# Performance work log

Measured on AMD Instinct MI355X. Metric: run time of the kernel, lower is better.

The kernel has to match this reference:

```python
import jax, jax.numpy as jnp
import numpy as np
import math

B, S, DIM, QK, HID = 20, 500, 300, 128, 600  # batch, seq, model dim, query_key_dim, hidden_dim
ROT = 32          # rotary dim = min(32, query_key_dim)
NB, MD = 32, 128  # T5 bias num_buckets, max_distance


def _layernorm(x, g, b, eps=1e-5):
    mu = jnp.mean(x, axis=-1, keepdims=True)
    var = jnp.var(x, axis=-1, keepdims=True)
    return (x - mu) / jnp.sqrt(var + eps) * g + b


def _rowquant(y, axis):
    # per-row (or per-col) symmetric int4-range quant used by the module:
    # scale = max|y|/15, clamp to [-15,15], truncate toward zero (torch .to(int8))
    s = jnp.max(jnp.abs(y), axis=axis, keepdims=True) / 15.0
    yq = jnp.trunc(jnp.clip(y / s, -15.0, 15.0))
    return yq, s


def _rotary(t):
    # rotary-embedding-torch: rotate first ROT features, interleaved pairs
    inv_freq = 1.0 / (10000.0 ** (jnp.arange(0, ROT, 2, dtype=jnp.float32) / ROT))  # [ROT/2]
    pos = jnp.arange(S, dtype=jnp.float32)
    freqs = jnp.repeat(pos[:, None] * inv_freq[None, :], 2, axis=-1)  # [S, ROT]
    cos, sin = jnp.cos(freqs), jnp.sin(freqs)
    tr, tp = t[..., :ROT], t[..., ROT:]
    x1, x2 = tr[..., 0::2], tr[..., 1::2]
    rot_half = jnp.stack([-x2, x1], axis=-1).reshape(tr.shape)
    return jnp.concatenate([tr * cos + rot_half * sin, tp], axis=-1)


def _t5_bias(rel_emb):
    # non-causal T5 relative position bucket, num_buckets=32 -> halved to 16
    pos = jnp.arange(S)
    n = -(pos[None, :] - pos[:, None])  # -(k_pos - q_pos)
    nb = NB // 2
    ret = (n < 0).astype(jnp.int32) * nb
    n = jnp.abs(n)
    max_exact = nb // 2
    is_small = n < max_exact
    n_safe = jnp.maximum(n, 1).astype(jnp.float32)
    val_large = max_exact + (jnp.log(n_safe / max_exact) / math.log(MD / max_exact) * (nb - max_exact)).astype(jnp.int32)
    val_large = jnp.minimum(val_large, nb - 1)
    bucket = ret + jnp.where(is_small, n, val_large)  # [S, S]
    return rel_emb[bucket, 0] * math.sqrt(QK)


def setup_inputs() -> dict:
    key = jax.random.key(0)
    ks = jax.random.split(key, 16)
    nrm = lambda i, shp, std=0.02: jax.random.normal(ks[i], shp, jnp.float32) * std
    uni = lambda i, shp, lo, hi: jax.random.uniform(ks[i], shp, jnp.float32, lo, hi)
    return {
        "x": jax.random.normal(ks[0], (B, S, DIM), jnp.float32),
        "norm_gamma": jnp.ones((DIM,), jnp.float32),
        "norm_beta": jnp.zeros((DIM,), jnp.float32),
        "Wh": nrm(1, (2 * HID, DIM)),
        "bh": jnp.zeros((2 * HID,), jnp.float32),
        "Wqk": nrm(2, (QK, DIM)),
        "bqk": jnp.zeros((QK,), jnp.float32),
        "os_gamma": nrm(3, (2, QK)),
        "os_beta": jnp.zeros((2, QK), jnp.float32),
        "Wo": nrm(4, (DIM, HID)),
        "bo": jnp.zeros((DIM,), jnp.float32),
        "rel_emb": nrm(5, (NB, 1), 0.1),
        "qk_s": uni(6, (DIM,), 0.5, 1.5),
        "hidden_s": uni(7, (DIM,), 0.5, 1.5),
        "out_s": uni(8, (HID,), 0.5, 1.5),
        "hidden_params": uni(9, (2 * HID,), 0.01, 0.05),
        "qk_params": uni(10, (QK,), 0.01, 0.05),
        "out_params": uni(11, (DIM,), 0.01, 0.05),
    }


def reference(x, norm_gamma, norm_beta, Wh, bh, Wqk, bqk, os_gamma, os_beta, Wo, bo,
              rel_emb, qk_s, hidden_s, out_s, hidden_params, qk_params, out_params):
    normed = _layernorm(x, norm_gamma, norm_beta)
    # token shift on first half of features
    half = DIM // 2
    x_shift = jnp.pad(normed[..., :half], ((0, 0), (1, 0), (0, 0)))[:, :S, :]
    normed = jnp.concatenate([x_shift, normed[..., half:]], axis=-1)

    # per-weight-column pre-scale then per-row int8 quant
    xq_q, sq = _rowquant(normed / qk_s, axis=-1)      # sq [B,S,1]
    xh_q, sh = _rowquant(normed / hidden_s, axis=-1)  # sh [B,S,1]

    # to_hidden: Linear + SiLU, then dequant outer(row_scale, hidden_params)
    v_gate = jax.nn.silu(xh_q @ Wh.T + bh) * (sh * hidden_params)  # [B,S,2*HID]
    v, gate = v_gate[..., :HID], v_gate[..., HID:]

    qk = jax.nn.silu(xq_q @ Wqk.T + bqk) * (sq * qk_params)  # [B,S,QK]
    q = qk * os_gamma[0] + os_beta[0]
    k = qk * os_gamma[1] + os_beta[1]
    q, k = _rotary(q), _rotary(k)

    qq, qs = _rowquant(q, axis=-1)
    kq, ks_ = _rowquant(k, axis=-1)
    sim = jnp.trunc(jnp.einsum('bid,bjd->bij', qq, kq)) * qs * jnp.swapaxes(ks_, 1, 2)
    sim = sim + _t5_bias(rel_emb)

    attn = jnp.square(jax.nn.relu(sim / S))
    aq, as_ = _rowquant(attn, axis=-1)  # as_ [B,S,1]
    vq, vs = _rowquant(v, axis=1)       # vs [B,1,HID] (per-column)
    out = jnp.trunc(jnp.einsum('bij,bjd->bid', aq, vq)) * as_ * vs  # [B,S,HID]

    out = out * gate / out_s
    oq, osc = _rowquant(out, axis=-1)
    out = (oq @ Wo.T + bo) * (osc * out_params)  # [B,S,DIM]
    return out + x
```

## Files before the change

kernel.cpp:

```cpp
#include <hip/hip_runtime.h>
#include <math.h>

#define B_   20
#define S_   500
#define DIM_ 300
#define QK_  128
#define HID_ 600
#define NROW (B_ * S_)

typedef int   v4i  __attribute__((ext_vector_type(4)));

__device__ __forceinline__ unsigned short f32_to_bf16(float f) {
  unsigned int u = __float_as_uint(f);
  unsigned int r = (u + 0x7FFFu + ((u >> 16) & 1u)) >> 16;
  return (unsigned short)r;
}
__device__ __forceinline__ float bf16_to_f32(unsigned short s) {
  return __uint_as_float(((unsigned int)s) << 16);
}

__device__ __forceinline__ float quant15(float y, float s) {
  return truncf(fminf(fmaxf(__fdiv_rn(y, s), -15.f), 15.f));
}

__global__ __launch_bounds__(256) void k_prep_ln(
    const float* __restrict__ x,
    const float* __restrict__ g, const float* __restrict__ b,
    const float* __restrict__ qk_s, const float* __restrict__ hidden_s,
    signed char* __restrict__ xq8, signed char* __restrict__ xh8,
    float* __restrict__ sq, float* __restrict__ sh,
    const float* __restrict__ rel_emb, float* __restrict__ dbias,
    const float* __restrict__ Wh, signed char* __restrict__ q1h, float* __restrict__ s1h,
    const float* __restrict__ Wo, signed char* __restrict__ q1o, float* __restrict__ s1o,
    const float* __restrict__ Wqk, signed char* __restrict__ q1k, float* __restrict__ s1k) {
  int blk = blockIdx.x;
  int tid = threadIdx.x;
  int lane = tid & 63;
  if (blk < 2500) {
    int row = blk * 4 + (tid >> 6);
    if (row >= NROW) return;
    bool hasp = (row % S_) > 0;
    const float* xr = x + (size_t)row * DIM_;
    const float* xpr = x + (size_t)(row - 1) * DIM_;
    float xc[5], xp[5];
    #pragma unroll
    for (int i = 0; i < 5; ++i) {
      int c = lane + i * 64;
      xc[i] = (c < DIM_) ? xr[c] : 0.f;
      xp[i] = (hasp && c < DIM_) ? xpr[c] : 0.f;
    }
    float sc = 0.f, sp = 0.f;
    #pragma unroll
    for (int i = 0; i < 5; ++i) { sc += xc[i]; sp += xp[i]; }
    #pragma unroll
    for (int off = 1; off < 64; off <<= 1) {
      sc += __shfl_xor(sc, off);
      sp += __shfl_xor(sp, off);
    }
    float mu_c = sc / (float)DIM_, mu_p = sp / (float)DIM_;
    float vc = 0.f, vp = 0.f;
    #pragma unroll
    for (int i = 0; i < 5; ++i) {
      int c = lane + i * 64;
      if (c < DIM_) {
        float dc = xc[i] - mu_c; vc += dc * dc;
        float dp = xp[i] - mu_p; vp += dp * dp;
      }
    }
    #pragma unroll
    for (int off = 1; off < 64; off <<= 1) {
      vc += __shfl_xor(vc, off);
      vp += __shfl_xor(vp, off);
    }
    float den_c = sqrtf(vc / (float)DIM_ + 1e-5f);
    float den_p = sqrtf(vp / (float)DIM_ + 1e-5f);
    float yq[5], yh[5];
    float mq = 0.f, mh = 0.f;
    #pragma unroll
    for (int i = 0; i < 5; ++i) {
      int c = lane + i * 64;
      if (c < DIM_) {
        float src;
        if (c < DIM_ / 2)
          src = hasp ? __fdiv_rn(xp[i] - mu_p, den_p) * g[c] + b[c] : 0.f;
        else
          src = __fdiv_rn(xc[i] - mu_c, den_c) * g[c] + b[c];
        yq[i] = __fdiv_rn(src, qk_s[c]);
        yh[i] = __fdiv_rn(src, hidden_s[c]);
        mq = fmaxf(mq, fabsf(yq[i]));
        mh = fmaxf(mh, fabsf(yh[i]));
      }
    }
    #pragma unroll
    for (int off = 1; off < 64; off <<= 1) {
      mq = fmaxf(mq, __shfl_xor(mq, off));
      mh = fmaxf(mh, __shfl_xor(mh, off));
    }
    float sqv = mq / 15.0f, shv = mh / 15.0f;
    if (lane == 0) { sq[row] = sqv; sh[row] = shv; }
    #pragma unroll
    for (int i = 0; i < 5; ++i) {
      int c = lane + i * 64;
      if (c < DIM_) {
        xq8[(size_t)row * 320 + c] = (signed char)quant15(yq[i], sqv);
        xh8[(size_t)row * 320 + c] = (signed char)quant15(yh[i], shv);
      } else if (c < 320) {
        xq8[(size_t)row * 320 + c] = 0;
        xh8[(size_t)row * 320 + c] = 0;
      }
    }
    return;
  }
  int jidx = (blk - 2500) * 4 + (tid >> 6);
  if (jidx >= 1744) return;
  if (jidx < 16) {
    int idx = jidx * 64 + lane;
    int dd = idx - 512;
    int ret = (dd < 0) ? 16 : 0;
    int n = dd < 0 ? -dd : dd;
    int v;
    if (n < 8)       v = n;
    else if (n < 12) v = 8;
    else if (n < 16) v = 9;
    else if (n < 23) v = 10;
    else if (n < 32) v = 11;
    else if (n < 46) v = 12;
    else if (n < 64) v = 13;
    else if (n < 91) v = 14;
    else             v = 15;
    dbias[idx] = __fmul_rn(rel_emb[ret + v], 11.313708498984761f);
    return;
  }
  const float* src; signed char* q1; float* s1;
  int j, C, CP;
  if (jidx < 1296)      { j = jidx - 16;   src = Wh;  q1 = q1h; s1 = s1h; C = DIM_; CP = 320; }
  else if (jidx < 1616) { j = jidx - 1296; src = Wo;  q1 = q1o; s1 = s1o; C = HID_; CP = 640; }
  else                  { j = jidx - 1616; src = Wqk; q1 = q1k; s1 = s1k; C = DIM_; CP = 320; }
  float m = 0.f;
  for (int k = lane; k < C; k += 64) m = fmaxf(m, fabsf(src[(size_t)j * C + k]));
  #pragma unroll
  for (int off = 1; off < 64; off <<= 1) m = fmaxf(m, __shfl_xor(m, off));
  float s1v = m / 127.0f;
  float s1inv = s1v > 0.f ? 1.0f / s1v : 0.f;
  if (lane == 0) s1[j] = s1v;
  for (int k = lane; k < CP; k += 64) {
    float wv = (k < C) ? src[(size_t)j * C + k] : 0.f;
    float q1f = fminf(fmaxf(rintf(wv * s1inv), -127.f), 127.f);
    q1[(size_t)j * CP + k] = (signed char)q1f;
  }
}

__global__ __launch_bounds__(512) void k_hidden(
    const signed char* __restrict__ xh8p, const float* __restrict__ sh,
    const signed char* __restrict__ q1h, const float* __restrict__ s1h,
    const float* __restrict__ bh, const float* __restrict__ hp,
    unsigned short* __restrict__ v16, unsigned short* __restrict__ gate16,
    int* __restrict__ vsmax) {
  int j0 = blockIdx.x * 64;
  int i0 = blockIdx.y * 256;
  int tid = threadIdx.x;
  int w = tid >> 6, l = tid & 63, g = l >> 4, ln = l & 15;
  int wm = w >> 1, wn = w & 1;
  __shared__ __align__(16) signed char smem[33792];
  signed char* a_lds  = smem;
  signed char* b1_lds = smem + 16384;
  unsigned short* st  = (unsigned short*)smem;

  int r0 = tid >> 2, ch0 = tid & 3;
  int r1 = r0 + 128;
  int koff0 = ((ch0 ^ ((r0 >> 1) & 3)) * 16);
  int koff1 = ((ch0 ^ ((r1 >> 1) & 3)) * 16);
  int ga0 = i0 + r0; if (ga0 >= NROW) ga0 = NROW - 1;
  int ga1 = i0 + r1; if (ga1 >= NROW) ga1 = NROW - 1;
  const signed char* srcA0 = xh8p + (size_t)ga0 * 320 + koff0;
  const signed char* srcA1 = xh8p + (size_t)ga1 * 320 + koff1;
  bool hasB = tid < 256;
  int br = (tid & 255) >> 2, bch = tid & 3;
  int bkoff = ((bch ^ ((br >> 1) & 3)) * 16);
  const signed char* srcB = q1h + (size_t)(j0 + br) * 320 + bkoff;

  v4i pa0 = *(const v4i*)srcA0;
  v4i pa1 = *(const v4i*)srcA1;
  v4i zero = {0, 0, 0, 0};
  v4i pb = hasB ? *(const v4i*)srcB : zero;

  int rxor = ((g ^ ((ln >> 1) & 3)) * 16);
  v4i acc1[4][2];
  #pragma unroll
  for (int sl = 0; sl < 4; ++sl)
    #pragma unroll
    for (int t = 0; t < 2; ++t) acc1[sl][t] = zero;

  for (int st_i = 0; st_i < 5; ++st_i) {
    *(v4i*)(a_lds + tid * 16)        = pa0;
    *(v4i*)(a_lds + 8192 + tid * 16) = pa1;
    if (hasB) *(v4i*)(b1_lds + tid * 16) = pb;
    __syncthreads();
    if (st_i < 4) {
      int k0 = (st_i + 1) * 64;
      pa0 = *(const v4i*)(srcA0 + k0);
      pa1 = *(const v4i*)(srcA1 + k0);
      if (hasB) pb = *(const v4i*)(srcB + k0);
    }
    v4i af[4];
    #pragma unroll
    for (int sl = 0; sl < 4; ++sl)
      af[sl] = *(const v4i*)(a_lds + (wm * 64 + sl * 16 + ln) * 64 + rxor);
    #pragma unroll
    for (int t = 0; t < 2; ++t) {
      int boff = (wn * 32 + t * 16 + ln) * 64 + rxor;
      v4i b1 = *(const v4i*)(b1_lds + boff);
      #pragma unroll
      for (int sl = 0; sl < 4; ++sl)
        acc1[sl][t] = __builtin_amdgcn_mfma_i32_16x16x64_i8(af[sl], b1, acc1[sl][t], 0, 0, 0);
    }
    __syncthreads();
  }
  int rbase = i0 + wm * 64;
  int b0 = rbase / S_;
  int bbound = (b0 + 1) * S_;
  int rtop = rbase + 63; if (rtop >= NROW) rtop = NROW - 1;
  int b1i = rtop / S_;
  #pragma unroll
  for (int t = 0; t < 2; ++t) {
    int col = j0 + wn * 32 + t * 16 + ln;
    int cl = wn * 32 + t * 16 + ln;
    if (col < 2 * HID_) {
      float s1v = s1h[col], bc = bh[col], hpc = hp[col];
      bool isv = col < HID_;
      float m0 = 0.f, m1 = 0.f;
      #pragma unroll
      for (int sl = 0; sl < 4; ++sl) {
        #pragma unroll
        for (int r = 0; r < 4; ++r) {
          int grow = rbase + sl * 16 + g * 4 + r;
          if (grow < NROW) {
            float z = s1v * (float)acc1[sl][t][r] + bc;
            float sig = 1.0f / (1.0f + __expf(-z));
            float val = __fmul_rn(z * sig, __fmul_rn(sh[grow], hpc));
            unsigned short hv = f32_to_bf16(val);
            st[(wm * 64 + sl * 16 + g * 4 + r) * 66 + cl] = hv;
            if (isv) {
              float vr = fabsf(bf16_to_f32(hv));
              if (grow < bbound) m0 = fmaxf(m0, vr);
              else               m1 = fmaxf(m1, vr);
            }
          }
        }
      }
      if (isv) {
        atomicMax(&vsmax[b0 * 640 + col], __float_as_int(m0));
        if (b1i != b0) atomicMax(&vsmax[b1i * 640 + col], __float_as_int(m1));
      }
    }
  }
  __syncthreads();
  for (int idx = tid; idx < 2048; idx += 512) {
    int r = idx >> 3, seg = idx & 7;
    int grow = i0 + r;
    int col0 = j0 + seg * 8;
    if (grow < NROW && col0 < 2 * HID_) {
      const unsigned int* sp = (const unsigned int*)(st + r * 66 + seg * 8);
      v4i pk;
      pk[0] = sp[0]; pk[1] = sp[1]; pk[2] = sp[2]; pk[3] = sp[3];
      if (col0 < HID_)
        *(v4i*)(v16 + (size_t)grow * HID_ + col0) = pk;
      else
        *(v4i*)(gate16 + (size_t)grow * HID_ + (col0 - HID_)) = pk;
    }
  }
}

__global__ __launch_bounds__(256) void k_qk(
    const signed char* __restrict__ xq8p, const float* __restrict__ sq,
    const signed char* __restrict__ q1k, const float* __restrict__ s1k,
    const float* __restrict__ bqk, const float* __restrict__ qkp,
    const float* __restrict__ osg, const float* __restrict__ osb,
    signed char* __restrict__ qq8, signed char* __restrict__ kq2,
    float* __restrict__ qs, float* __restrict__ ks) {
  int i0 = blockIdx.x * 64;
  int tid = threadIdx.x;
  int w = tid >> 6, l = tid & 63, g = l >> 4, ln = l & 15;
  __shared__ __align__(16) signed char a_lds[64 * 64];
  __shared__ __align__(16) signed char b1_lds[128 * 64];
  __shared__ float freqs[32];
  if (tid < 32) {
    double e = (double)(tid & ~1) / 32.0;
    freqs[tid] = (float)(1.0 / pow(10000.0, e));
  }
  int arow = tid >> 2;
  int xorb = (((tid & 3) ^ ((tid >> 3) & 3)) * 16);
  int ga = i0 + arow; if (ga >= NROW) ga = NROW - 1;
  const signed char* srcA   = xq8p + (size_t)ga * 320 + xorb;
  const signed char* srcB1a = q1k + (size_t)arow * 320 + xorb;
  const signed char* srcB1b = q1k + (size_t)(64 + arow) * 320 + xorb;
  v4i pa   = *(const v4i*)srcA;
  v4i pb1a = *(const v4i*)srcB1a, pb1b = *(const v4i*)srcB1b;
  int rxor = ((g ^ ((ln >> 1) & 3)) * 16);
  v4i acc1[8];
  v4i zero = {0, 0, 0, 0};
  #pragma unroll
  for (int t = 0; t < 8; ++t) acc1[t] = zero;
  for (int st = 0; st < 5; ++st) {
    *(v4i*)(a_lds + tid * 16)         = pa;
    *(v4i*)(b1_lds + tid * 16)        = pb1a;
    *(v4i*)(b1_lds + 4096 + tid * 16) = pb1b;
    __syncthreads();
    if (st < 4) {
      int k0 = (st + 1) * 64;
      pa   = *(const v4i*)(srcA + k0);
      pb1a = *(const v4i*)(srcB1a + k0);
      pb1b = *(const v4i*)(srcB1b + k0);
    }
    v4i af = *(const v4i*)(a_lds + (w * 16 + ln) * 64 + rxor);
    #pragma unroll
    for (int t = 0; t < 8; ++t) {
      int boff = (t * 16 + ln) * 64 + rxor;
      v4i b1 = *(const v4i*)(b1_lds + boff);
      acc1[t] = __builtin_amdgcn_mfma_i32_16x16x64_i8(af, b1, acc1[t], 0, 0, 0);
    }
    __syncthreads();
  }
  int growr[4]; float sqr[4];
  #pragma unroll
  for (int r = 0; r < 4; ++r) {
    growr[r] = i0 + w * 16 + g * 4 + r;
    int gc = growr[r] < NROW ? growr[r] : NROW - 1;
    sqr[r] = sq[gc];
  }
  float qv[8][4], kv[8][4];
  #pragma unroll
  for (int t = 0; t < 8; ++t) {
    int c = t * 16 + ln;
    float s1v = s1k[c], bc = bqk[c], qkpc = qkp[c];
    float g0 = osg[c], g1 = osg[QK_ + c], b0 = osb[c], b1v = osb[QK_ + c];
    #pragma unroll
    for (int r = 0; r < 4; ++r) {
      float z = s1v * (float)acc1[t][r] + bc;
      float sig = 1.0f / (1.0f + expf(-z));
      float qkv = __fmul_rn(z * sig, __fmul_rn(sqr[r], qkpc));
      qv[t][r] = __fadd_rn(__fmul_rn(qkv, g0), b0);
      kv[t][r] = __fadd_rn(__fmul_rn(qkv, g1), b1v);
    }
  }
  #pragma unroll
  for (int t = 0; t < 2; ++t) {
    float inv = freqs[t * 16 + ln];
    #pragma unroll
    for (int r = 0; r < 4; ++r) {
      int pos = growr[r] % S_;
      float fr = __fmul_rn((float)pos, inv);
      float cs = cosf(fr), sn = sinf(fr);
      float qo = __shfl_xor(qv[t][r], 1);
      float ko = __shfl_xor(kv[t][r], 1);
      float rq = ((ln & 1) == 0) ? -qo : qo;
      float rk = ((ln & 1) == 0) ? -ko : ko;
      qv[t][r] = __fadd_rn(__fmul_rn(qv[t][r], cs), __fmul_rn(rq, sn));
      kv[t][r] = __fadd_rn(__fmul_rn(kv[t][r], cs), __fmul_rn(rk, sn));
    }
  }
  float qsv[4], ksv[4];
  #pragma unroll
  for (int r = 0; r < 4; ++r) {
    float mq = 0.f, mk = 0.f;
    #pragma unroll
    for (int t = 0; t < 8; ++t) {
      mq = fmaxf(mq, fabsf(qv[t][r]));
      mk = fmaxf(mk, fabsf(kv[t][r]));
    }
    #pragma unroll
    for (int off = 1; off < 16; off <<= 1) {
      mq = fmaxf(mq, __shfl_xor(mq, off));
      mk = fmaxf(mk, __shfl_xor(mk, off));
    }
    qsv[r] = mq / 15.0f; ksv[r] = mk / 15.0f;
    if (ln == 0 && growr[r] < NROW) { qs[growr[r]] = qsv[r]; ks[growr[r]] = ksv[r]; }
  }
  #pragma unroll
  for (int t = 0; t < 8; ++t) {
    int c = t * 16 + ln;
    #pragma unroll
    for (int r = 0; r < 4; ++r) {
      if (growr[r] < NROW) {
        qq8[(size_t)growr[r] * QK_ + c] = (signed char)quant15(qv[t][r], qsv[r]);
        int bb = growr[r] / S_, ss = growr[r] % S_;
        kq2[(((size_t)bb * 2 + (c >> 6)) * 512 + ss) * 64 + (c & 63)] =
            (signed char)quant15(kv[t][r], ksv[r]);
      }
    }
  }
}

__global__ __launch_bounds__(512) void k_simpv(
    const signed char* __restrict__ qq8, const signed char* __restrict__ kq2,
    const float* __restrict__ qs, const float* __restrict__ ks,
    const float* __restrict__ dbias,
    const signed char* __restrict__ vqt2, const float* __restrict__ vg,
    const unsigned short* __restrict__ gate16,
    signed char* __restrict__ oq8, float* __restrict__ osc) {
  int i0 = blockIdx.x * 16;
  int b = blockIdx.y;
  int tid = threadIdx.x;
  int w = tid >> 6, l = tid & 63, g = l >> 4, ln = l & 15;
  __shared__ __align__(16) signed char q_lds[16 * 144];
  __shared__ __align__(16) signed char p_lds[16 * 528];
  __shared__ float db[1024];
  __shared__ int rowmax[16];
  if (tid < 128) {
    int r = tid >> 3, ww = tid & 7;
    *(v4i*)(q_lds + r * 144 + ww * 16) =
        *(const v4i*)(qq8 + ((size_t)(b * S_ + i0 + r)) * QK_ + ww * 16);
  }
  for (int idx = tid; idx < 1024; idx += 512) db[idx] = dbias[idx];
  if (tid < 16) rowmax[tid] = 0;
  __syncthreads();
  v4i acc[4];
  v4i zero = {0, 0, 0, 0};
  #pragma unroll
  for (int t = 0; t < 4; ++t) acc[t] = zero;
  #pragma unroll
  for (int kk = 0; kk < 2; ++kk) {
    v4i afrag = *(const v4i*)(q_lds + ln * 144 + kk * 64 + g * 16);
    #pragma unroll
    for (int t = 0; t < 4; ++t) {
      int j0 = (w * 4 + t) * 16;
      v4i bfrag = *(const v4i*)(kq2 + (((size_t)b * 2 + kk) * 512 + j0 + ln) * 64 + g * 16);
      acc[t] = __builtin_amdgcn_mfma_i32_16x16x64_i8(afrag, bfrag, acc[t], 0, 0, 0);
    }
  }
  float qsr[4];
  #pragma unroll
  for (int r = 0; r < 4; ++r) qsr[r] = qs[b * S_ + i0 + g * 4 + r];
  float rm[4] = {0.f, 0.f, 0.f, 0.f};
  #pragma unroll
  for (int t = 0; t < 4; ++t) {
    int j = (w * 4 + t) * 16 + ln;
    bool jv = j < S_;
    float ksv = ks[b * S_ + j];
    #pragma unroll
    for (int r = 0; r < 4; ++r) {
      int ip = i0 + g * 4 + r;
      float av = 0.f;
      if (jv) {
        float simv = __fmul_rn(__fmul_rn((float)acc[t][r], qsr[r]), ksv);
        simv = __fadd_rn(simv, db[ip - j + 512]);
        float rr = fmaxf(__fmul_rn(simv, 0.002f), 0.f);
        av = __fmul_rn(rr, rr);
      }
      rm[r] = fmaxf(rm[r], av);
      acc[t][r] = __float_as_int(av);
    }
  }
  #pragma unroll
  for (int r = 0; r < 4; ++r) atomicMax(&rowmax[g * 4 + r], __float_as_int(rm[r]));
  __syncthreads();
  float asr[4], rinv[4];
  #pragma unroll
  for (int r = 0; r < 4; ++r) {
    asr[r] = __int_as_float(rowmax[g * 4 + r]) / 15.0f;
    rinv[r] = __fdiv_rn(1.0f, asr[r]);
  }
  #pragma unroll
  for (int t = 0; t < 4; ++t) {
    int j = (w * 4 + t) * 16 + ln;
    #pragma unroll
    for (int r = 0; r < 4; ++r) {
      float y = __int_as_float(acc[t][r]);
      float q = truncf(fminf(fmaxf(__fmul_rn(y, rinv[r]), -15.f), 15.f));
      p_lds[(g * 4 + r) * 528 + j] = (signed char)q;
    }
  }
  __syncthreads();
  if (tid < 16) rowmax[tid] = 0;
  __syncthreads();
  v4i pacc[5];
  #pragma unroll
  for (int t = 0; t < 5; ++t) pacc[t] = zero;
  for (int kk = 0; kk < 8; ++kk) {
    v4i afrag = *(const v4i*)(p_lds + ln * 528 + kk * 64 + g * 16);
    const signed char* bbase = vqt2 + (((size_t)b * 8 + kk) * 640) * 64 + g * 16;
    #pragma unroll
    for (int t = 0; t < 5; ++t) {
      int d = (w * 5 + t) * 16 + ln;
      v4i bfrag = *(const v4i*)(bbase + (size_t)d * 64);
      pacc[t] = __builtin_amdgcn_mfma_i32_16x16x64_i8(afrag, bfrag, pacc[t], 0, 0, 0);
    }
  }
  float rm2[4] = {0.f, 0.f, 0.f, 0.f};
  #pragma unroll
  for (int t = 0; t < 5; ++t) {
    int d = (w * 5 + t) * 16 + ln;
    bool dv = d < HID_;
    float vgv = vg[b * 640 + d];
    #pragma unroll
    for (int r = 0; r < 4; ++r) {
      float o = 0.f;
      if (dv) {
        float gt = bf16_to_f32(gate16[((size_t)(b * S_ + i0 + g * 4 + r)) * HID_ + d]);
        o = __fmul_rn(__fmul_rn(__fmul_rn((float)pacc[t][r], asr[r]), vgv), gt);
      }
      rm2[r] = fmaxf(rm2[r], fabsf(o));
      pacc[t][r] = __float_as_int(o);
    }
  }
  #pragma unroll
  for (int r = 0; r < 4; ++r) atomicMax(&rowmax[g * 4 + r], __float_as_int(rm2[r]));
  __syncthreads();
  float orinv[4];
  #pragma unroll
  for (int r = 0; r < 4; ++r) {
    float osr = __int_as_float(rowmax[g * 4 + r]) / 15.0f;
    orinv[r] = __fdiv_rn(1.0f, osr);
  }
  #pragma unroll
  for (int t = 0; t < 5; ++t) {
    int d = (w * 5 + t) * 16 + ln;
    #pragma unroll
    for (int r = 0; r < 4; ++r) {
      int il = i0 + g * 4 + r;
      if (il < S_) {
        signed char valc = 0;
        if (d < HID_) {
          float q = truncf(fminf(fmaxf(
              __fmul_rn(__int_as_float(pacc[t][r]), orinv[r]), -15.f), 15.f));
          valc = (signed char)q;
        }
        oq8[((size_t)b * S_ + il) * 640 + d] = valc;
      }
    }
  }
  if (tid < 16 && i0 + tid < S_)
    osc[b * S_ + i0 + tid] = __int_as_float(rowmax[tid]) / 15.0f;
}

__global__ __launch_bounds__(256) void k_vq2(const unsigned short* __restrict__ v16,
                                             const int* __restrict__ vsmax,
                                             const float* __restrict__ out_s,
                                             signed char* __restrict__ vqt2,
                                             float* __restrict__ vg) {
  int b = blockIdx.z;
  int s0 = blockIdx.x * 64;
  int d0 = blockIdx.y * 64;
  __shared__ float tile[64][65];
  int tid = threadIdx.x;
  int dj = tid & 63, si4 = tid >> 6;
  #pragma unroll
  for (int it = 0; it < 16; ++it) {
    int s = s0 + it * 4 + si4;
    int d = d0 + dj;
    float val = 0.f;
    if (s < S_ && d < HID_) val = bf16_to_f32(v16[((size_t)b * S_ + s) * HID_ + d]);
    tile[it * 4 + si4][dj] = val;
  }
  if (blockIdx.x == 0 && tid < 64) {
    int d = d0 + tid;
    float vsv = __int_as_float(vsmax[b * 640 + d]) / 15.0f;
    vg[b * 640 + d] = (d < HID_) ? __fdiv_rn(vsv, out_s[d]) : 0.f;
  }
  __syncthreads();
  int dd = tid >> 2, seg = tid & 3;
  int d = d0 + dd;
  int kk = s0 >> 6;
  v4i pack = {0, 0, 0, 0};
  if (d < HID_) {
    float vsv = __int_as_float(vsmax[b * 640 + d]) / 15.0f;
    signed char* pc = (signed char*)&pack;
    #pragma unroll
    for (int e = 0; e < 16; ++e)
      pc[e] = (signed char)quant15(tile[seg * 16 + e][dd], vsv);
  }
  *(v4i*)(vqt2 + ((((size_t)b * 8 + kk) * 640) + d) * 64 + seg * 16) = pack;
}

__global__ __launch_bounds__(256) void k_final(
    const signed char* __restrict__ oq8p, const float* __restrict__ osc,
    const signed char* __restrict__ q1o, const float* __restrict__ s1o,
    const float* __restrict__ bo, const float* __restrict__ op,
    const float* __restrict__ x, float* __restrict__ out) {
  int i0 = blockIdx.x * 128;
  int j0 = blockIdx.y * 64;
  int tid = threadIdx.x;
  int w = tid >> 6, l = tid & 63, g = l >> 4, ln = l & 15;
  int wm = w >> 1, wn = w & 1;
  __shared__ __align__(16) signed char a_lds[128 * 64];
  __shared__ __align__(16) signed char b1_lds[64 * 64];

  int arow0 = tid >> 2;
  int xorb = (((tid & 3) ^ ((tid >> 3) & 3)) * 16);
  int ga0 = i0 + arow0;       if (ga0 >= NROW) ga0 = NROW - 1;
  int ga1 = i0 + arow0 + 64;  if (ga1 >= NROW) ga1 = NROW - 1;
  int gcol = j0 + arow0;
  const signed char* srcA0 = oq8p + (size_t)ga0 * 640 + xorb;
  const signed char* srcA1 = oq8p + (size_t)ga1 * 640 + xorb;
  const signed char* srcB1 = q1o + (size_t)gcol * 640 + xorb;

  v4i pa0 = *(const v4i*)(srcA0);
  v4i pa1 = *(const v4i*)(srcA1);
  v4i pb1 = *(const v4i*)(srcB1);

  int rxor = ((g ^ ((ln >> 1) & 3)) * 16);
  v4i acc1[4][2];
  v4i zero = {0, 0, 0, 0};
  #pragma unroll
  for (int sl = 0; sl < 4; ++sl)
    #pragma unroll
    for (int t = 0; t < 2; ++t) acc1[sl][t] = zero;

  for (int st = 0; st < 10; ++st) {
    *(v4i*)(a_lds + tid * 16)        = pa0;
    *(v4i*)(a_lds + 4096 + tid * 16) = pa1;
    *(v4i*)(b1_lds + tid * 16)       = pb1;
    __syncthreads();
    if (st < 9) {
      int k0 = (st + 1) * 64;
      pa0 = *(const v4i*)(srcA0 + k0);
      pa1 = *(const v4i*)(srcA1 + k0);
      pb1 = *(const v4i*)(srcB1 + k0);
    }
    v4i af[4];
    #pragma unroll
    for (int sl = 0; sl < 4; ++sl)
      af[sl] = *(const v4i*)(a_lds + (wm * 64 + sl * 16 + ln) * 64 + rxor);
    #pragma unroll
    for (int t = 0; t < 2; ++t) {
      int boff = (wn * 32 + t * 16 + ln) * 64 + rxor;
      v4i b1 = *(const v4i*)(b1_lds + boff);
      #pragma unroll
      for (int sl = 0; sl < 4; ++sl)
        acc1[sl][t] = __builtin_amdgcn_mfma_i32_16x16x64_i8(af[sl], b1, acc1[sl][t], 0, 0, 0);
    }
    __syncthreads();
  }
  #pragma unroll
  for (int t = 0; t < 2; ++t) {
    int col = j0 + wn * 32 + t * 16 + ln;
    if (col < DIM_) {
      float s1v = s1o[col], bc = bo[col], opc = op[col];
      #pragma unroll
      for (int sl = 0; sl < 4; ++sl) {
        #pragma unroll
        for (int r = 0; r < 4; ++r) {
          int grow = i0 + wm * 64 + sl * 16 + g * 4 + r;
          if (grow < NROW) {
            float z = s1v * (float)acc1[sl][t][r] + bc;
            float tval = __fmul_rn(osc[grow], opc);
            out[(size_t)grow * DIM_ + col] =
                __fmul_rn(z, tval) + x[(size_t)grow * DIM_ + col];
          }
        }
      }
    }
  }
}

extern "C" void kernel_launch(void* const* d_in, const int* in_sizes, int n_in,
                              void* d_out, int out_size, void* d_ws, size_t ws_size,
                              hipStream_t stream) {
  const float* x        = (const float*)d_in[0];
  const float* ng       = (const float*)d_in[1];
  const float* nbt      = (const float*)d_in[2];
  const float* Wh       = (const float*)d_in[3];
  const float* bh       = (const float*)d_in[4];
  const float* Wqk      = (const float*)d_in[5];
  const float* bqk      = (const float*)d_in[6];
  const float* osg      = (const float*)d_in[7];
  const float* osb      = (const float*)d_in[8];
  const float* Wo       = (const float*)d_in[9];
  const float* bo       = (const float*)d_in[10];
  const float* rel      = (const float*)d_in[11];
  const float* qk_s     = (const float*)d_in[12];
  const float* hidden_s = (const float*)d_in[13];
  const float* out_s    = (const float*)d_in[14];
  const float* hp       = (const float*)d_in[15];
  const float* qkp      = (const float*)d_in[16];
  const float* op       = (const float*)d_in[17];
  float* out = (float*)d_out;

  char* ws = (char*)d_ws;
  size_t off = 0;
  auto alloc = [&](size_t bytes) {
    void* p = ws + off;
    off += (bytes + 255) & ~(size_t)255;
    return p;
  };
  signed char* xq8    = (signed char*)alloc((size_t)(NROW + 128) * 320);
  signed char* xh8    = (signed char*)alloc((size_t)(NROW + 256) * 320);
  float*       sq     = (float*)      alloc((size_t)(NROW + 256) * 4);
  float*       sh     = (float*)      alloc((size_t)(NROW + 256) * 4);
  unsigned short* v16   = (unsigned short*)alloc((size_t)(NROW + 256) * HID_ * 2);
  unsigned short* gate16= (unsigned short*)alloc((size_t)(NROW + 256) * HID_ * 2);
  signed char* qq8    = (signed char*)alloc((size_t)(NROW + 128) * QK_);
  signed char* kq2    = (signed char*)alloc((size_t)B_ * 2 * 512 * 64);
  float*       qs     = (float*)      alloc((size_t)(NROW + 128) * 4);
  float*       ks     = (float*)      alloc((size_t)(NROW + 128) * 4);
  signed char* vqt2   = (signed char*)alloc((size_t)B_ * 8 * 640 * 64);
  float*       vg     = (float*)      alloc((size_t)B_ * 640 * 4);
  int*         vsmax  = (int*)        alloc((size_t)B_ * 640 * 4);
  signed char* oq8    = (signed char*)alloc((size_t)(NROW + 128) * 640);
  float*       osc    = (float*)      alloc((size_t)(NROW + 128) * 4);
  float*       dbias  = (float*)      alloc((size_t)1024 * 4);
  signed char* q1h    = (signed char*)alloc((size_t)1280 * 320);
  float*       s1h    = (float*)      alloc((size_t)1280 * 4);
  signed char* q1o    = (signed char*)alloc((size_t)320 * 640);
  float*       s1o    = (float*)      alloc((size_t)320 * 4);
  signed char* q1k    = (signed char*)alloc((size_t)QK_ * 320);
  float*       s1k    = (float*)      alloc((size_t)QK_ * 4);


  k_prep_ln<<<2936, 256, 0, stream>>>(x, ng, nbt, qk_s, hidden_s, xq8, xh8, sq, sh,
                                      rel, dbias, Wh, q1h, s1h, Wo, q1o, s1o,
                                      Wqk, q1k, s1k);
  k_hidden<<<dim3(19, 40), 512, 0, stream>>>(xh8, sh, q1h, s1h, bh, hp,
                                             v16, gate16, vsmax);
  k_qk<<<157, 256, 0, stream>>>(xq8, sq, q1k, s1k, bqk, qkp, osg, osb,
                                qq8, kq2, qs, ks);
  k_vq2<<<dim3(8, 10, B_), 256, 0, stream>>>(v16, vsmax, out_s, vqt2, vg);
  k_simpv<<<dim3(32, B_), 512, 0, stream>>>(qq8, kq2, qs, ks, dbias, vqt2, vg,
                                            gate16, oq8, osc);
  k_final<<<dim3(79, 5), 256, 0, stream>>>(oq8, osc, q1o, s1o, bo, op, x, out);
}
```

Before: 124.7 us.

## Merge V quantization into QK kernel and double simpv row tile

```diff
diff --git a/kernel.cpp b/kernel.cpp
--- a/kernel.cpp
+++ b/kernel.cpp
@@ -271,15 +271,55 @@
   }
 }
 
-__global__ __launch_bounds__(256) void k_qk(
+__global__ __launch_bounds__(256) void k_qkv(
     const signed char* __restrict__ xq8p, const float* __restrict__ sq,
     const signed char* __restrict__ q1k, const float* __restrict__ s1k,
     const float* __restrict__ bqk, const float* __restrict__ qkp,
     const float* __restrict__ osg, const float* __restrict__ osb,
     signed char* __restrict__ qq8, signed char* __restrict__ kq2,
-    float* __restrict__ qs, float* __restrict__ ks) {
-  int i0 = blockIdx.x * 64;
+    float* __restrict__ qs, float* __restrict__ ks,
+    const unsigned short* __restrict__ v16, const int* __restrict__ vsmax,
+    const float* __restrict__ out_s,
+    signed char* __restrict__ vqt2, float* __restrict__ vg) {
+  int blk = blockIdx.x;
   int tid = threadIdx.x;
+  if (blk >= 157) {
+    int idx = blk - 157;
+    int b = idx / 80;
+    int rem = idx % 80;
+    int s0 = (rem % 8) * 64;
+    int d0 = (rem / 8) * 64;
+    __shared__ float tile[64][65];
+    int dj = tid & 63, si4 = tid >> 6;
+    #pragma unroll
+    for (int it = 0; it < 16; ++it) {
+      int s = s0 + it * 4 + si4;
+      int d = d0 + dj;
+      float val = 0.f;
+      if (s < S_ && d < HID_) val = bf16_to_f32(v16[((size_t)b * S_ + s) * HID_ + d]);
+      tile[it * 4 + si4][dj] = val;
+    }
+    if (s0 == 0 && tid < 64) {
+      int d = d0 + tid;
+      float vsv = __int_as_float(vsmax[b * 640 + d]) / 15.0f;
+      vg[b * 640 + d] = (d < HID_) ? __fdiv_rn(vsv, out_s[d]) : 0.f;
+    }
+    __syncthreads();
+    int dd = tid >> 2, seg = tid & 3;
+    int d = d0 + dd;
+    int kk = s0 >> 6;
+    v4i pack = {0, 0, 0, 0};
+    if (d < HID_) {
+      float vsv = __int_as_float(vsmax[b * 640 + d]) / 15.0f;
+      signed char* pc = (signed char*)&pack;
+      #pragma unroll
+      for (int e = 0; e < 16; ++e)
+        pc[e] = (signed char)quant15(tile[seg * 16 + e][dd], vsv);
+    }
+    *(v4i*)(vqt2 + ((((size_t)b * 8 + kk) * 640) + d) * 64 + seg * 16) = pack;
+    return;
+  }
+  int i0 = blk * 64;
   int w = tid >> 6, l = tid & 63, g = l >> 4, ln = l & 15;
   __shared__ __align__(16) signed char a_lds[64 * 64];
   __shared__ __align__(16) signed char b1_lds[128 * 64];
@@ -398,48 +438,50 @@
     const signed char* __restrict__ vqt2, const float* __restrict__ vg,
     const unsigned short* __restrict__ gate16,
     signed char* __restrict__ oq8, float* __restrict__ osc) {
-  int i0 = blockIdx.x * 16;
+  int i0 = blockIdx.x * 32;
   int b = blockIdx.y;
   int tid = threadIdx.x;
   int w = tid >> 6, l = tid & 63, g = l >> 4, ln = l & 15;
-  __shared__ __align__(16) signed char q_lds[16 * 144];
-  __shared__ __align__(16) signed char p_lds[16 * 528];
+  int rs = w >> 2;
+  int wq = w & 3;
+  __shared__ __align__(16) signed char q_lds[32 * 144];
+  __shared__ __align__(16) signed char p_lds[32 * 528];
   __shared__ float db[1024];
-  __shared__ int rowmax[16];
-  if (tid < 128) {
+  __shared__ int rowmax[32];
+  if (tid < 256) {
     int r = tid >> 3, ww = tid & 7;
     *(v4i*)(q_lds + r * 144 + ww * 16) =
         *(const v4i*)(qq8 + ((size_t)(b * S_ + i0 + r)) * QK_ + ww * 16);
   }
   for (int idx = tid; idx < 1024; idx += 512) db[idx] = dbias[idx];
-  if (tid < 16) rowmax[tid] = 0;
+  if (tid < 32) rowmax[tid] = 0;
   __syncthreads();
-  v4i acc[4];
+  v4i acc[8];
   v4i zero = {0, 0, 0, 0};
   #pragma unroll
-  for (int t = 0; t < 4; ++t) acc[t] = zero;
+  for (int t = 0; t < 8; ++t) acc[t] = zero;
   #pragma unroll
   for (int kk = 0; kk < 2; ++kk) {
-    v4i afrag = *(const v4i*)(q_lds + ln * 144 + kk * 64 + g * 16);
-    #pragma unroll
-    for (int t = 0; t < 4; ++t) {
-      int j0 = (w * 4 + t) * 16;
+    v4i afrag = *(const v4i*)(q_lds + (rs * 16 + ln) * 144 + kk * 64 + g * 16);
+    #pragma unroll
+    for (int t = 0; t < 8; ++t) {
+      int j0 = (wq * 8 + t) * 16;
       v4i bfrag = *(const v4i*)(kq2 + (((size_t)b * 2 + kk) * 512 + j0 + ln) * 64 + g * 16);
       acc[t] = __builtin_amdgcn_mfma_i32_16x16x64_i8(afrag, bfrag, acc[t], 0, 0, 0);
     }
   }
   float qsr[4];
   #pragma unroll
-  for (int r = 0; r < 4; ++r) qsr[r] = qs[b * S_ + i0 + g * 4 + r];
+  for (int r = 0; r < 4; ++r) qsr[r] = qs[b * S_ + i0 + rs * 16 + g * 4 + r];
   float rm[4] = {0.f, 0.f, 0.f, 0.f};
   #pragma unroll
-  for (int t = 0; t < 4; ++t) {
-    int j = (w * 4 + t) * 16 + ln;
+  for (int t = 0; t < 8; ++t) {
+    int j = (wq * 8 + t) * 16 + ln;
     bool jv = j < S_;
     float ksv = ks[b * S_ + j];
     #pragma unroll
     for (int r = 0; r < 4; ++r) {
-      int ip = i0 + g * 4 + r;
+      int ip = i0 + rs * 16 + g * 4 + r;
       float av = 0.f;
       if (jv) {
         float simv = __fmul_rn(__fmul_rn((float)acc[t][r], qsr[r]), ksv);
@@ -452,51 +494,53 @@
     }
   }
   #pragma unroll
-  for (int r = 0; r < 4; ++r) atomicMax(&rowmax[g * 4 + r], __float_as_int(rm[r]));
+  for (int r = 0; r < 4; ++r)
+    atomicMax(&rowmax[rs * 16 + g * 4 + r], __float_as_int(rm[r]));
   __syncthreads();
   float asr[4], rinv[4];
   #pragma unroll
   for (int r = 0; r < 4; ++r) {
-    asr[r] = __int_as_float(rowmax[g * 4 + r]) / 15.0f;
+    asr[r] = __int_as_float(rowmax[rs * 16 + g * 4 + r]) / 15.0f;
     rinv[r] = __fdiv_rn(1.0f, asr[r]);
   }
   #pragma unroll
-  for (int t = 0; t < 4; ++t) {
-    int j = (w * 4 + t) * 16 + ln;
+  for (int t = 0; t < 8; ++t) {
+    int j = (wq * 8 + t) * 16 + ln;
     #pragma unroll
     for (int r = 0; r < 4; ++r) {
       float y = __int_as_float(acc[t][r]);
       float q = truncf(fminf(fmaxf(__fmul_rn(y, rinv[r]), -15.f), 15.f));
-      p_lds[(g * 4 + r) * 528 + j] = (signed char)q;
+      p_lds[(rs * 16 + g * 4 + r) * 528 + j] = (signed char)q;
     }
   }
   __syncthreads();
-  if (tid < 16) rowmax[tid] = 0;
+  if (tid < 32) rowmax[tid] = 0;
   __syncthreads();
-  v4i pacc[5];
-  #pragma unroll
-  for (int t = 0; t < 5; ++t) pacc[t] = zero;
+  v4i pacc[10];
+  #pragma unroll
+  for (int t = 0; t < 10; ++t) pacc[t] = zero;
   for (int kk = 0; kk < 8; ++kk) {
-    v4i afrag = *(const v4i*)(p_lds + ln * 528 + kk * 64 + g * 16);
+    v4i afrag = *(const v4i*)(p_lds + (rs * 16 + ln) * 528 + kk * 64 + g * 16);
     const signed char* bbase = vqt2 + (((size_t)b * 8 + kk) * 640) * 64 + g * 16;
     #pragma unroll
-    for (int t = 0; t < 5; ++t) {
-      int d = (w * 5 + t) * 16 + ln;
+    for (int t = 0; t < 10; ++t) {
+      int d = (wq * 10 + t) * 16 + ln;
       v4i bfrag = *(const v4i*)(bbase + (size_t)d * 64);
       pacc[t] = __builtin_amdgcn_mfma_i32_16x16x64_i8(afrag, bfrag, pacc[t], 0, 0, 0);
     }
   }
   float rm2[4] = {0.f, 0.f, 0.f, 0.f};
   #pragma unroll
-  for (int t = 0; t < 5; ++t) {
-    int d = (w * 5 + t) * 16 + ln;
+  for (int t = 0; t < 10; ++t) {
+    int d = (wq * 10 + t) * 16 + ln;
     bool dv = d < HID_;
     float vgv = vg[b * 640 + d];
     #pragma unroll
     for (int r = 0; r < 4; ++r) {
       float o = 0.f;
       if (dv) {
-        float gt = bf16_to_f32(gate16[((size_t)(b * S_ + i0 + g * 4 + r)) * HID_ + d]);
+        float gt = bf16_to_f32(
+            gate16[((size_t)(b * S_ + i0 + rs * 16 + g * 4 + r)) * HID_ + d]);
         o = __fmul_rn(__fmul_rn(__fmul_rn((float)pacc[t][r], asr[r]), vgv), gt);
       }
       rm2[r] = fmaxf(rm2[r], fabsf(o));
@@ -504,20 +548,21 @@
     }
   }
   #pragma unroll
-  for (int r = 0; r < 4; ++r) atomicMax(&rowmax[g * 4 + r], __float_as_int(rm2[r]));
+  for (int r = 0; r < 4; ++r)
+    atomicMax(&rowmax[rs * 16 + g * 4 + r], __float_as_int(rm2[r]));
   __syncthreads();
   float orinv[4];
   #pragma unroll
   for (int r = 0; r < 4; ++r) {
-    float osr = __int_as_float(rowmax[g * 4 + r]) / 15.0f;
+    float osr = __int_as_float(rowmax[rs * 16 + g * 4 + r]) / 15.0f;
     orinv[r] = __fdiv_rn(1.0f, osr);
   }
   #pragma unroll
-  for (int t = 0; t < 5; ++t) {
-    int d = (w * 5 + t) * 16 + ln;
+  for (int t = 0; t < 10; ++t) {
+    int d = (wq * 10 + t) * 16 + ln;
     #pragma unroll
     for (int r = 0; r < 4; ++r) {
-      int il = i0 + g * 4 + r;
+      int il = i0 + rs * 16 + g * 4 + r;
       if (il < S_) {
         signed char valc = 0;
         if (d < HID_) {
@@ -529,47 +574,8 @@
       }
     }
   }
-  if (tid < 16 && i0 + tid < S_)
+  if (tid < 32 && i0 + tid < S_)
     osc[b * S_ + i0 + tid] = __int_as_float(rowmax[tid]) / 15.0f;
-}
-
-__global__ __launch_bounds__(256) void k_vq2(const unsigned short* __restrict__ v16,
-                                             const int* __restrict__ vsmax,
-                                             const float* __restrict__ out_s,
-                                             signed char* __restrict__ vqt2,
-                                             float* __restrict__ vg) {
-  int b = blockIdx.z;
-  int s0 = blockIdx.x * 64;
-  int d0 = blockIdx.y * 64;
-  __shared__ float tile[64][65];
-  int tid = threadIdx.x;
-  int dj = tid & 63, si4 = tid >> 6;
-  #pragma unroll
-  for (int it = 0; it < 16; ++it) {
-    int s = s0 + it * 4 + si4;
-    int d = d0 + dj;
-    float val = 0.f;
-    if (s < S_ && d < HID_) val = bf16_to_f32(v16[((size_t)b * S_ + s) * HID_ + d]);
-    tile[it * 4 + si4][dj] = val;
-  }
-  if (blockIdx.x == 0 && tid < 64) {
-    int d = d0 + tid;
-    float vsv = __int_as_float(vsmax[b * 640 + d]) / 15.0f;
-    vg[b * 640 + d] = (d < HID_) ? __fdiv_rn(vsv, out_s[d]) : 0.f;
-  }
-  __syncthreads();
-  int dd = tid >> 2, seg = tid & 3;
-  int d = d0 + dd;
-  int kk = s0 >> 6;
-  v4i pack = {0, 0, 0, 0};
-  if (d < HID_) {
-    float vsv = __int_as_float(vsmax[b * 640 + d]) / 15.0f;
-    signed char* pc = (signed char*)&pack;
-    #pragma unroll
-    for (int e = 0; e < 16; ++e)
-      pc[e] = (signed char)quant15(tile[seg * 16 + e][dd], vsv);
-  }
-  *(v4i*)(vqt2 + ((((size_t)b * 8 + kk) * 640) + d) * 64 + seg * 16) = pack;
 }
 
 __global__ __launch_bounds__(256) void k_final(
@@ -712,10 +718,10 @@
                                       Wqk, q1k, s1k);
   k_hidden<<<dim3(19, 40), 512, 0, stream>>>(xh8, sh, q1h, s1h, bh, hp,
                                              v16, gate16, vsmax);
-  k_qk<<<157, 256, 0, stream>>>(xq8, sq, q1k, s1k, bqk, qkp, osg, osb,
-                                qq8, kq2, qs, ks);
-  k_vq2<<<dim3(8, 10, B_), 256, 0, stream>>>(v16, vsmax, out_s, vqt2, vg);
-  k_simpv<<<dim3(32, B_), 512, 0, stream>>>(qq8, kq2, qs, ks, dbias, vqt2, vg,
+  k_qkv<<<157 + 1600, 256, 0, stream>>>(xq8, sq, q1k, s1k, bqk, qkp, osg, osb,
+                                        qq8, kq2, qs, ks,
+                                        v16, vsmax, out_s, vqt2, vg);
+  k_simpv<<<dim3(16, B_), 512, 0, stream>>>(qq8, kq2, qs, ks, dbias, vqt2, vg,
                                             gate16, oq8, osc);
   k_final<<<dim3(79, 5), 256, 0, stream>>>(oq8, osc, q1o, s1o, bo, op, x, out);
 }
```

Result: slower. 128.4 us (+2.9%).
